# Performance work log

Measured on AMD Instinct MI355X. Metric: run time of the kernel, lower is better.

The kernel has to match this reference:

```python
import jax, jax.numpy as jnp
import numpy as np

N = 50000      # nodes
E = 640000     # edges (before self loops)
IN = 128       # in_channels
H = 4          # heads (layer 1)
C = 64         # hidden_channels per head
OUT = 64       # out_channels
SLOPE = 0.2    # PyG GATConv default negative_slope


def setup_inputs() -> dict:
    key = jax.random.key(0)
    ks = jax.random.split(key, 12)
    x = jax.random.normal(ks[0], (N, IN), dtype=jnp.float32)
    edge_src = jax.random.randint(ks[1], (E,), 0, N, dtype=jnp.int32)
    edge_dst = jax.random.randint(ks[2], (E,), 0, N, dtype=jnp.int32)
    # Layer 1 params: Linear IN -> H*C, attention vectors a_src/a_dst [H, C], bias [H*C]
    W1 = jax.random.normal(ks[3], (IN, H * C), dtype=jnp.float32) / np.sqrt(IN)
    att_src1 = jax.random.normal(ks[4], (H, C), dtype=jnp.float32) / np.sqrt(C)
    att_dst1 = jax.random.normal(ks[5], (H, C), dtype=jnp.float32) / np.sqrt(C)
    b1 = jnp.zeros((H * C,), dtype=jnp.float32)
    # Layer 2 params: Linear H*C -> OUT, 1 head
    W2 = jax.random.normal(ks[6], (H * C, OUT), dtype=jnp.float32) / np.sqrt(H * C)
    att_src2 = jax.random.normal(ks[7], (1, OUT), dtype=jnp.float32) / np.sqrt(OUT)
    att_dst2 = jax.random.normal(ks[8], (1, OUT), dtype=jnp.float32) / np.sqrt(OUT)
    b2 = jnp.zeros((OUT,), dtype=jnp.float32)
    return {"x": x, "W1": W1, "att_src1": att_src1, "att_dst1": att_dst1, "b1": b1,
            "W2": W2, "att_src2": att_src2, "att_dst2": att_dst2, "b2": b2,
            "edge_src": edge_src, "edge_dst": edge_dst}


def gat_conv(x, src, dst, W, a_src, a_dst, b, heads, ch):
    """PyG GATConv (concat=True): gather -> LeakyReLU attention -> per-dst softmax -> scatter-add."""
    n = x.shape[0]
    h = (x @ W).reshape(n, heads, ch)                  # [N, H, C]
    al_s = jnp.sum(h * a_src, axis=-1)                 # [N, H] node-level src attention term
    al_d = jnp.sum(h * a_dst, axis=-1)                 # [N, H]
    e = jax.nn.leaky_relu(al_s[src] + al_d[dst], SLOPE)  # [E, H] edge scores
    m = jax.ops.segment_max(e, dst, num_segments=n)    # stable per-dst softmax
    ex = jnp.exp(e - m[dst])
    den = jax.ops.segment_sum(ex, dst, num_segments=n)
    alpha = ex / den[dst]                              # [E, H]
    msg = h[src] * alpha[:, :, None]                   # [E, H, C]
    out = jax.ops.segment_sum(msg, dst, num_segments=n)  # [N, H, C]
    return out.reshape(n, heads * ch) + b


def reference(x, W1, att_src1, att_dst1, b1, W2, att_src2, att_dst2, b2, edge_src, edge_dst):
    # PyG GATConv default add_self_loops=True
    loops = jnp.arange(N, dtype=edge_src.dtype)
    src = jnp.concatenate([edge_src, loops])
    dst = jnp.concatenate([edge_dst, loops])
    h = gat_conv(x, src, dst, W1, att_src1, att_dst1, b1, H, C)
    h = jax.nn.elu(h)                                  # F.elu; dropout p=0 -> no-op
    out = gat_conv(h, src, dst, W2, att_src2, att_dst2, b2, 1, OUT)
    return out
```

## Files before the change

### kernel.cpp

```cpp
#include <hip/hip_runtime.h>
#include <hip/hip_bf16.h>
#include <cstdint>
#include <cstddef>

#define N_NODES 50000
#define N_EDGES 640000
#define ET (N_EDGES + N_NODES)
#define IN_CH 128
#define H1 4
#define HC1 256
#define OUT_CH 64
#define SLOPE 0.2f
#define SCAN_NBLK ((N_NODES + 255) / 256)
#define XW (N_NODES * IN_CH / 8)
#define W1N (IN_CH * HC1)
#define W2N (HC1 * OUT_CH)
#define CONVB ((XW + W1N + W2N + 255) / 256)
#define EDGEB ((ET + 255) / 256)
#define MT ((N_NODES + 63) / 64)
#define G1B (4 * MT)

typedef __attribute__((ext_vector_type(8))) short short8;
typedef __attribute__((ext_vector_type(4))) float floatx4;

__device__ __forceinline__ float bf2f(unsigned short u) {
    return __uint_as_float(((unsigned)u) << 16);
}
__device__ __forceinline__ unsigned short f2bf(float f) {
    unsigned u = __float_as_uint(f);
    unsigned r = 0x7fffu + ((u >> 16) & 1u);
    return (unsigned short)((u + r) >> 16);
}
__device__ __forceinline__ float ldf(const void* p, size_t i, bool f32) {
    return f32 ? ((const float*)p)[i] : bf2f(((const unsigned short*)p)[i]);
}

__global__ __launch_bounds__(256) void init_all(
    const unsigned short* __restrict__ x, unsigned* __restrict__ flag,
    int* __restrict__ counts, int* __restrict__ state)
{
    int b = blockIdx.x;
    if (b < SCAN_NBLK) {
        int i = b * 256 + threadIdx.x;
        if (i < N_NODES) counts[i] = 0;
    } else {
        int t = threadIdx.x;
        if (t < 64) {
            int bad = 0;
            #pragma unroll
            for (int r = 0; r < 4; ++r) {
                float v = bf2f(x[r * 64 + t]);
                if (!(v == v) || fabsf(v) > 1e4f) bad = 1;
            }
            unsigned long long m = __ballot(bad != 0);
            if (t == 0) *flag = (m != 0ull) ? 1u : 0u;
        } else if (t == 64) {
            state[0] = 0; state[1] = 0;
        }
    }
}

__global__ __launch_bounds__(256) void conv_count(
    const void* __restrict__ x, const void* __restrict__ W1,
    const void* __restrict__ W2, const unsigned* __restrict__ flag,
    unsigned short* __restrict__ x16,
    unsigned short* __restrict__ Wt1, unsigned short* __restrict__ Wt2,
    const int* __restrict__ edst, int* __restrict__ counts,
    int* __restrict__ epos)
{
    int b = blockIdx.x;
    if (b < CONVB) {
        int i = b * 256 + threadIdx.x;
        const bool f32 = (*flag != 0);
        if (i < XW) {
            size_t off = (size_t)i * 8;
            uint4 st;
            if (f32) {
                const float* xp = (const float*)x + off;
                float4 a = *(const float4*)xp;
                float4 c = *(const float4*)(xp + 4);
                st.x = (unsigned)f2bf(a.x) | ((unsigned)f2bf(a.y) << 16);
                st.y = (unsigned)f2bf(a.z) | ((unsigned)f2bf(a.w) << 16);
                st.z = (unsigned)f2bf(c.x) | ((unsigned)f2bf(c.y) << 16);
                st.w = (unsigned)f2bf(c.z) | ((unsigned)f2bf(c.w) << 16);
            } else {
                st = *(const uint4*)((const unsigned short*)x + off);
            }
            *(uint4*)(x16 + off) = st;
        } else if (i < XW + W1N) {
            int j = i - XW;
            int n = j / IN_CH, k = j % IN_CH;
            Wt1[j] = f2bf(ldf(W1, (size_t)k * HC1 + n, f32));
        } else if (i < XW + W1N + W2N) {
            int j = i - XW - W1N;
            int n = j / HC1, k = j % HC1;
            Wt2[j] = f2bf(ldf(W2, (size_t)k * OUT_CH + n, f32));
        }
    } else {
        int i = (b - CONVB) * 256 + threadIdx.x;
        if (i < ET) {
            int d = (i < N_EDGES) ? edst[i] : (i - N_EDGES);
            epos[i] = atomicAdd(&counts[d], 1);
        }
    }
}

__global__ __launch_bounds__(256) void scan_onepass(
    const int* __restrict__ counts, int* __restrict__ rowptr,
    int* __restrict__ bsum, int* __restrict__ boff, int* __restrict__ state)
{
    __shared__ int s[256];
    const int t = threadIdx.x, b = blockIdx.x;
    const int i = b * 256 + t;
    int v = (i < N_NODES) ? counts[i] : 0;
    s[t] = v;
    __syncthreads();
    #pragma unroll
    for (int off = 1; off < 256; off <<= 1) {
        int u = (t >= off) ? s[t - off] : 0;
        __syncthreads();
        s[t] += u;
        __syncthreads();
    }
    const int incl = s[t];
    if (t == 255) {
        __hip_atomic_store(&bsum[b], incl, __ATOMIC_RELAXED, __HIP_MEMORY_SCOPE_AGENT);
        __hip_atomic_fetch_add(&state[0], 1, __ATOMIC_ACQ_REL, __HIP_MEMORY_SCOPE_AGENT);
    }
    if (b == 0) {
        if (t == 0) {
            while (__hip_atomic_load(&state[0], __ATOMIC_ACQUIRE, __HIP_MEMORY_SCOPE_AGENT) < SCAN_NBLK)
                __builtin_amdgcn_s_sleep(8);
        }
        __syncthreads();
        int w = (t < SCAN_NBLK)
              ? __hip_atomic_load(&bsum[t], __ATOMIC_RELAXED, __HIP_MEMORY_SCOPE_AGENT) : 0;
        s[t] = w;
        __syncthreads();
        #pragma unroll
        for (int off = 1; off < 256; off <<= 1) {
            int u = (t >= off) ? s[t - off] : 0;
            __syncthreads();
            s[t] += u;
            __syncthreads();
        }
        if (t < SCAN_NBLK)
            __hip_atomic_store(&boff[t], s[t] - w, __ATOMIC_RELAXED, __HIP_MEMORY_SCOPE_AGENT);
        __syncthreads();
        if (t == 0)
            __hip_atomic_store(&state[1], 1, __ATOMIC_RELEASE, __HIP_MEMORY_SCOPE_AGENT);
    }
    if (t == 0) {
        while (__hip_atomic_load(&state[1], __ATOMIC_ACQUIRE, __HIP_MEMORY_SCOPE_AGENT) == 0)
            __builtin_amdgcn_s_sleep(8);
    }
    __syncthreads();
    int off0 = __hip_atomic_load(&boff[b], __ATOMIC_RELAXED, __HIP_MEMORY_SCOPE_AGENT);
    if (i < N_NODES)
        rowptr[i] = off0 + incl - v;
    if (i == 0) rowptr[N_NODES] = ET;
}

template <int KK>
__device__ __forceinline__ void gemm_body(
    const unsigned short* __restrict__ A, const unsigned short* __restrict__ Bt,
    const void* __restrict__ avs, const void* __restrict__ avd,
    const unsigned* __restrict__ flag, unsigned short* __restrict__ C,
    float* __restrict__ als, float* __restrict__ ald,
    int M, int N, int bx, int by)
{
    const int tid = threadIdx.x;
    const int m0 = by * 64, n0 = bx * 64;
    const int w = tid >> 6, lane = tid & 63;
    const int ln = lane & 15, quad = lane >> 4;
    const int m_frag = m0 + w * 16 + ln;
    floatx4 acc[4] = {{0.f,0.f,0.f,0.f},{0.f,0.f,0.f,0.f},{0.f,0.f,0.f,0.f},{0.f,0.f,0.f,0.f}};

    #pragma unroll
    for (int ks = 0; ks < KK / 32; ++ks) {
        const int kbase = ks * 32 + quad * 8;
        short8 a;
        if (m_frag < M) {
            a = *(const short8*)(A + (size_t)m_frag * KK + kbase);
        } else {
            #pragma unroll
            for (int j = 0; j < 8; ++j) a[j] = 0;
        }
        #pragma unroll
        for (int sub = 0; sub < 4; ++sub) {
            short8 b = *(const short8*)(Bt + (size_t)(n0 + sub * 16 + ln) * KK + kbase);
            acc[sub] = __builtin_amdgcn_mfma_f32_16x16x32_bf16(a, b, acc[sub], 0, 0, 0);
        }
    }

    #pragma unroll
    for (int sub = 0; sub < 4; ++sub) {
        #pragma unroll
        for (int r = 0; r < 4; ++r) {
            int m = m0 + w * 16 + quad * 4 + r;
            if (m < M)
                C[(size_t)m * N + n0 + sub * 16 + ln] = f2bf(acc[sub][r]);
        }
    }

    const bool f32in = (*flag != 0);
    float as[4], av[4];
    #pragma unroll
    for (int sub = 0; sub < 4; ++sub) {
        as[sub] = ldf(avs, n0 + sub * 16 + ln, f32in);
        av[sub] = ldf(avd, n0 + sub * 16 + ln, f32in);
    }
    const int Hh = N >> 6;
    #pragma unroll
    for (int r = 0; r < 4; ++r) {
        float ps = 0.f, pd = 0.f;
        #pragma unroll
        for (int sub = 0; sub < 4; ++sub) {
            ps += acc[sub][r] * as[sub];
            pd += acc[sub][r] * av[sub];
        }
        #pragma unroll
        for (int off = 1; off < 16; off <<= 1) {
            ps += __shfl_xor(ps, off, 64);
            pd += __shfl_xor(pd, off, 64);
        }
        int m = m0 + w * 16 + quad * 4 + r;
        if (ln == 0 && m < M) {
            als[(size_t)m * Hh + bx] = ps;
            ald[(size_t)m * Hh + bx] = pd;
        }
    }
}

__global__ __launch_bounds__(256) void gemm1_fill(
    const unsigned short* __restrict__ x16, const unsigned short* __restrict__ Wt1,
    const void* __restrict__ as1, const void* __restrict__ ad1,
    const unsigned* __restrict__ flag, unsigned short* __restrict__ h16,
    float* __restrict__ als, float* __restrict__ ald,
    const int* __restrict__ esrc, const int* __restrict__ edst,
    const int* __restrict__ rowptr, const int* __restrict__ epos,
    int* __restrict__ ecsr)
{
    int b = blockIdx.x;
    if (b < G1B) {
        gemm_body<IN_CH>(x16, Wt1, as1, ad1, flag, h16, als, ald,
                         N_NODES, HC1, b & 3, b >> 2);
    } else {
        int i = (b - G1B) * 256 + threadIdx.x;
        if (i < ET) {
            int s = (i < N_EDGES) ? esrc[i] : (i - N_EDGES);
            int d = (i < N_EDGES) ? edst[i] : (i - N_EDGES);
            ecsr[rowptr[d] + epos[i]] = s;
        }
    }
}

__global__ __launch_bounds__(256) void gemm2(
    const unsigned short* __restrict__ xo16, const unsigned short* __restrict__ Wt2,
    const void* __restrict__ as2, const void* __restrict__ ad2,
    const unsigned* __restrict__ flag, unsigned short* __restrict__ h2,
    float* __restrict__ als, float* __restrict__ ald)
{
    gemm_body<HC1>(xo16, Wt2, as2, ad2, flag, h2, als, ald,
                   N_NODES, OUT_CH, 0, blockIdx.x);
}

__global__ __launch_bounds__(256) void agg_node1(
    const int* __restrict__ rowptr, const int* __restrict__ ecsr,
    const unsigned short* __restrict__ h, const float* __restrict__ als,
    const float* __restrict__ ald, const void* __restrict__ bias,
    const unsigned* __restrict__ flag, unsigned short* __restrict__ out)
{
    int wave = (blockIdx.x * blockDim.x + threadIdx.x) >> 6;
    int lane = threadIdx.x & 63;
    if (wave >= N_NODES) return;
    const int d = wave;
    const int hg = lane >> 4;
    const int c0 = (lane & 15) << 2;
    const int lo = rowptr[d], hi = rowptr[d + 1];
    const float ad = ald[d * H1 + hg];

    float acc0 = 0.f, acc1 = 0.f, acc2 = 0.f, acc3 = 0.f, den = 0.f;

    int e = lo;
    for (; e + 3 < hi; e += 4) {
        int s0 = ecsr[e], s1 = ecsr[e + 1], s2 = ecsr[e + 2], s3 = ecsr[e + 3];
        uint2 q0 = *(const uint2*)(h + (size_t)s0 * HC1 + hg * 64 + c0);
        uint2 q1 = *(const uint2*)(h + (size_t)s1 * HC1 + hg * 64 + c0);
        uint2 q2 = *(const uint2*)(h + (size_t)s2 * HC1 + hg * 64 + c0);
        uint2 q3 = *(const uint2*)(h + (size_t)s3 * HC1 + hg * 64 + c0);
        float t0 = als[s0 * H1 + hg] + ad;
        float t1 = als[s1 * H1 + hg] + ad;
        float t2 = als[s2 * H1 + hg] + ad;
        float t3 = als[s3 * H1 + hg] + ad;
        t0 = (t0 > 0.f) ? t0 : SLOPE * t0;
        t1 = (t1 > 0.f) ? t1 : SLOPE * t1;
        t2 = (t2 > 0.f) ? t2 : SLOPE * t2;
        t3 = (t3 > 0.f) ? t3 : SLOPE * t3;
        float p0 = __expf(t0), p1 = __expf(t1), p2 = __expf(t2), p3 = __expf(t3);
        den += (p0 + p1) + (p2 + p3);
        acc0 += p0 * __uint_as_float(q0.x << 16)         + p1 * __uint_as_float(q1.x << 16)
              + p2 * __uint_as_float(q2.x << 16)         + p3 * __uint_as_float(q3.x << 16);
        acc1 += p0 * __uint_as_float(q0.x & 0xffff0000u) + p1 * __uint_as_float(q1.x & 0xffff0000u)
              + p2 * __uint_as_float(q2.x & 0xffff0000u) + p3 * __uint_as_float(q3.x & 0xffff0000u);
        acc2 += p0 * __uint_as_float(q0.y << 16)         + p1 * __uint_as_float(q1.y << 16)
              + p2 * __uint_as_float(q2.y << 16)         + p3 * __uint_as_float(q3.y << 16);
        acc3 += p0 * __uint_as_float(q0.y & 0xffff0000u) + p1 * __uint_as_float(q1.y & 0xffff0000u)
              + p2 * __uint_as_float(q2.y & 0xffff0000u) + p3 * __uint_as_float(q3.y & 0xffff0000u);
    }
    for (; e < hi; ++e) {
        int s0 = ecsr[e];
        uint2 q0 = *(const uint2*)(h + (size_t)s0 * HC1 + hg * 64 + c0);
        float t0 = als[s0 * H1 + hg] + ad;
        t0 = (t0 > 0.f) ? t0 : SLOPE * t0;
        float p0 = __expf(t0);
        den += p0;
        acc0 += p0 * __uint_as_float(q0.x << 16);
        acc1 += p0 * __uint_as_float(q0.x & 0xffff0000u);
        acc2 += p0 * __uint_as_float(q0.y << 16);
        acc3 += p0 * __uint_as_float(q0.y & 0xffff0000u);
    }

    const bool f32in = (*flag != 0);
    const float inv = 1.f / den;
    float v0 = acc0 * inv + ldf(bias, hg * 64 + c0 + 0, f32in);
    float v1 = acc1 * inv + ldf(bias, hg * 64 + c0 + 1, f32in);
    float v2 = acc2 * inv + ldf(bias, hg * 64 + c0 + 2, f32in);
    float v3 = acc3 * inv + ldf(bias, hg * 64 + c0 + 3, f32in);
    v0 = (v0 > 0.f) ? v0 : (__expf(v0) - 1.f);
    v1 = (v1 > 0.f) ? v1 : (__expf(v1) - 1.f);
    v2 = (v2 > 0.f) ? v2 : (__expf(v2) - 1.f);
    v3 = (v3 > 0.f) ? v3 : (__expf(v3) - 1.f);
    uint2 st;
    st.x = (unsigned)f2bf(v0) | ((unsigned)f2bf(v1) << 16);
    st.y = (unsigned)f2bf(v2) | ((unsigned)f2bf(v3) << 16);
    *(uint2*)(out + (size_t)d * HC1 + hg * 64 + c0) = st;
}

__global__ __launch_bounds__(256) void agg_node2(
    const int* __restrict__ rowptr, const int* __restrict__ ecsr,
    const unsigned short* __restrict__ h, const float* __restrict__ als,
    const float* __restrict__ ald, const void* __restrict__ bias,
    const unsigned* __restrict__ flag, float* __restrict__ out)
{
    int wave = (blockIdx.x * blockDim.x + threadIdx.x) >> 6;
    int lane = threadIdx.x & 63;
    if (wave >= N_NODES) return;
    const int d = wave;
    const int eg = lane >> 3;
    const int c0 = (lane & 7) << 3;
    const int lo = rowptr[d], hi = rowptr[d + 1];
    const float ad = ald[d];

    float acc[8];
    #pragma unroll
    for (int j = 0; j < 8; ++j) acc[j] = 0.f;
    float den = 0.f;

    for (int eb = lo; eb < hi; eb += 8) {
        int e = eb + eg;
        if (e < hi) {
            int s = ecsr[e];
            uint4 q = *(const uint4*)(h + (size_t)s * OUT_CH + c0);
            float t = als[s] + ad;
            t = (t > 0.f) ? t : SLOPE * t;
            float p = __expf(t);
            den += p;
            acc[0] += p * __uint_as_float(q.x << 16);
            acc[1] += p * __uint_as_float(q.x & 0xffff0000u);
            acc[2] += p * __uint_as_float(q.y << 16);
            acc[3] += p * __uint_as_float(q.y & 0xffff0000u);
            acc[4] += p * __uint_as_float(q.z << 16);
            acc[5] += p * __uint_as_float(q.z & 0xffff0000u);
            acc[6] += p * __uint_as_float(q.w << 16);
            acc[7] += p * __uint_as_float(q.w & 0xffff0000u);
        }
    }
    #pragma unroll
    for (int off = 8; off <= 32; off <<= 1) {
        den += __shfl_xor(den, off, 64);
        #pragma unroll
        for (int j = 0; j < 8; ++j) acc[j] += __shfl_xor(acc[j], off, 64);
    }
    if (lane < 8) {
        const bool f32in = (*flag != 0);
        const float inv = 1.f / den;
        float4 v0, v1;
        v0.x = acc[0] * inv + ldf(bias, c0 + 0, f32in);
        v0.y = acc[1] * inv + ldf(bias, c0 + 1, f32in);
        v0.z = acc[2] * inv + ldf(bias, c0 + 2, f32in);
        v0.w = acc[3] * inv + ldf(bias, c0 + 3, f32in);
        v1.x = acc[4] * inv + ldf(bias, c0 + 4, f32in);
        v1.y = acc[5] * inv + ldf(bias, c0 + 5, f32in);
        v1.z = acc[6] * inv + ldf(bias, c0 + 6, f32in);
        v1.w = acc[7] * inv + ldf(bias, c0 + 7, f32in);
        *(float4*)(out + (size_t)d * OUT_CH + c0) = v0;
        *(float4*)(out + (size_t)d * OUT_CH + c0 + 4) = v1;
    }
}

extern "C" void kernel_launch(void* const* d_in, const int* in_sizes, int n_in,
                              void* d_out, int out_size, void* d_ws, size_t ws_size,
                              hipStream_t stream)
{
    const void* x   = d_in[0];
    const void* W1  = d_in[1];
    const void* as1 = d_in[2];
    const void* ad1 = d_in[3];
    const void* b1  = d_in[4];
    const void* W2  = d_in[5];
    const void* as2 = d_in[6];
    const void* ad2 = d_in[7];
    const void* b2  = d_in[8];
    const int* esrc = (const int*)d_in[9];
    const int* edst = (const int*)d_in[10];
    float* out = (float*)d_out;

    char* base = (char*)d_ws;
    const size_t MB = 1024 * 1024;
    unsigned short* x16  = (unsigned short*)(base);
    unsigned short* h16  = (unsigned short*)(base + 13 * MB);
    unsigned short* xo16 = (unsigned short*)(base + 39 * MB);
    unsigned short* h2   = (unsigned short*)(base + 65 * MB);
    float* als    = (float*)(base + 72 * MB);
    float* ald    = (float*)(base + 73 * MB);
    unsigned short* Wt1 = (unsigned short*)(base + 74 * MB);
    unsigned short* Wt2 = (unsigned short*)(base + 75 * MB);
    int* counts   = (int*)(base + 76 * MB);
    int* rowptr   = (int*)(base + 77 * MB);
    int* ecsr     = (int*)(base + 79 * MB);
    int* bsum     = (int*)(base + 82 * MB);
    int* boff     = bsum + 256;
    int* state    = boff + 256;
    unsigned* flag = (unsigned*)(base + 83 * MB);
    int* epos     = (int*)(base + 84 * MB);

    const int BLK = 256;
    const int node_wave_blocks = (N_NODES * 64 + BLK - 1) / BLK;

    init_all<<<SCAN_NBLK + 1, BLK, 0, stream>>>(
        (const unsigned short*)x, flag, counts, state);

    conv_count<<<CONVB + EDGEB, BLK, 0, stream>>>(
        x, W1, W2, flag, x16, Wt1, Wt2, edst, counts, epos);

    scan_onepass<<<SCAN_NBLK, BLK, 0, stream>>>(
        counts, rowptr, bsum, boff, state);

    gemm1_fill<<<G1B + EDGEB, BLK, 0, stream>>>(
        x16, Wt1, as1, ad1, flag, h16, als, ald, esrc, edst, rowptr, epos, ecsr);

    agg_node1<<<node_wave_blocks, BLK, 0, stream>>>(
        rowptr, ecsr, h16, als, ald, b1, flag, xo16);

    gemm2<<<MT, BLK, 0, stream>>>(xo16, Wt2, as2, ad2, flag, h2, als, ald);

    agg_node2<<<node_wave_blocks, BLK, 0, stream>>>(
        rowptr, ecsr, h2, als, ald, b2, flag, out);
}
```

Before: 286.1 us.

## Pad CSR rows to multiples of 8 with dummy node, prefetch indices in aggregation

Each node's CSR segment is padded up to a multiple of 8 edges, and the padding points at a dummy node whose features are zero and whose source attention score is -1e30, so its softmax weight is zero. The aggregation kernels can then drop tail loops and bounds checks, load indices as aligned int4 vectors, and prefetch the next batch of indices. The layer-1 GEMM now computes all 256 output columns per block (16 sub-tiles) instead of splitting them across 4 blocks, and layers 1 and 2 get separate attention buffers. The cost is extra padded edges (up to 7 per node, with gathers of the dummy row), a larger accumulator footprint in the GEMM, and a fill pass that writes the padding entries.

Measured after the change: 291.8 us. About the same (+2.0%).

```diff
diff --git a/kernel.cpp b/kernel.cpp
--- a/kernel.cpp
+++ b/kernel.cpp
@@ -18,7 +18,8 @@
 #define CONVB ((XW + W1N + W2N + 255) / 256)
 #define EDGEB ((ET + 255) / 256)
 #define MT ((N_NODES + 63) / 64)
-#define G1B (4 * MT)
+#define PADB SCAN_NBLK
+#define DUMMY N_NODES
 
 typedef __attribute__((ext_vector_type(8))) short short8;
 typedef __attribute__((ext_vector_type(4))) float floatx4;
@@ -37,7 +38,9 @@
 
 __global__ __launch_bounds__(256) void init_all(
     const unsigned short* __restrict__ x, unsigned* __restrict__ flag,
-    int* __restrict__ counts, int* __restrict__ state)
+    int* __restrict__ counts, int* __restrict__ state,
+    unsigned short* __restrict__ h16, unsigned short* __restrict__ h2,
+    float* __restrict__ als1, float* __restrict__ als2)
 {
     int b = blockIdx.x;
     if (b < SCAN_NBLK) {
@@ -56,6 +59,15 @@
             if (t == 0) *flag = (m != 0ull) ? 1u : 0u;
         } else if (t == 64) {
             state[0] = 0; state[1] = 0;
+        } else if (t >= 128 && t < 192) {
+            uint2 z; z.x = 0u; z.y = 0u;
+            *((uint2*)(h16 + (size_t)DUMMY * HC1) + (t - 128)) = z;
+        } else if (t >= 192 && t < 224) {
+            ((unsigned*)(h2 + (size_t)DUMMY * OUT_CH))[t - 192] = 0u;
+        } else if (t >= 224 && t < 228) {
+            als1[(size_t)DUMMY * H1 + (t - 224)] = -1e30f;
+        } else if (t == 228) {
+            als2[DUMMY] = -1e30f;
         }
     }
 }
@@ -112,7 +124,7 @@
     __shared__ int s[256];
     const int t = threadIdx.x, b = blockIdx.x;
     const int i = b * 256 + t;
-    int v = (i < N_NODES) ? counts[i] : 0;
+    int v = (i < N_NODES) ? ((counts[i] + 7) & ~7) : 0;
     s[t] = v;
     __syncthreads();
     #pragma unroll
@@ -158,10 +170,10 @@
     int off0 = __hip_atomic_load(&boff[b], __ATOMIC_RELAXED, __HIP_MEMORY_SCOPE_AGENT);
     if (i < N_NODES)
         rowptr[i] = off0 + incl - v;
-    if (i == 0) rowptr[N_NODES] = ET;
-}
-
-template <int KK>
+    if (i == N_NODES - 1) rowptr[N_NODES] = off0 + incl;
+}
+
+template <int KK, int NSUB>
 __device__ __forceinline__ void gemm_body(
     const unsigned short* __restrict__ A, const unsigned short* __restrict__ Bt,
     const void* __restrict__ avs, const void* __restrict__ avd,
@@ -170,13 +182,16 @@
     int M, int N, int bx, int by)
 {
     const int tid = threadIdx.x;
-    const int m0 = by * 64, n0 = bx * 64;
+    const int m0 = by * 64, n0 = bx * (NSUB * 16);
     const int w = tid >> 6, lane = tid & 63;
     const int ln = lane & 15, quad = lane >> 4;
     const int m_frag = m0 + w * 16 + ln;
-    floatx4 acc[4] = {{0.f,0.f,0.f,0.f},{0.f,0.f,0.f,0.f},{0.f,0.f,0.f,0.f},{0.f,0.f,0.f,0.f}};
-
-    #pragma unroll
+    floatx4 acc[NSUB];
+    #pragma unroll
+    for (int sub = 0; sub < NSUB; ++sub)
+        acc[sub] = (floatx4){0.f, 0.f, 0.f, 0.f};
+
+    #pragma unroll 2
     for (int ks = 0; ks < KK / 32; ++ks) {
         const int kbase = ks * 32 + quad * 8;
         short8 a;
@@ -187,14 +202,14 @@
             for (int j = 0; j < 8; ++j) a[j] = 0;
         }
         #pragma unroll
-        for (int sub = 0; sub < 4; ++sub) {
+        for (int sub = 0; sub < NSUB; ++sub) {
             short8 b = *(const short8*)(Bt + (size_t)(n0 + sub * 16 + ln) * KK + kbase);
             acc[sub] = __builtin_amdgcn_mfma_f32_16x16x32_bf16(a, b, acc[sub], 0, 0, 0);
         }
     }
 
     #pragma unroll
-    for (int sub = 0; sub < 4; ++sub) {
+    for (int sub = 0; sub < NSUB; ++sub) {
         #pragma unroll
         for (int r = 0; r < 4; ++r) {
             int m = m0 + w * 16 + quad * 4 + r;
@@ -204,30 +219,33 @@
     }
 
     const bool f32in = (*flag != 0);
-    float as[4], av[4];
-    #pragma unroll
-    for (int sub = 0; sub < 4; ++sub) {
+    float as[NSUB], av[NSUB];
+    #pragma unroll
+    for (int sub = 0; sub < NSUB; ++sub) {
         as[sub] = ldf(avs, n0 + sub * 16 + ln, f32in);
         av[sub] = ldf(avd, n0 + sub * 16 + ln, f32in);
     }
     const int Hh = N >> 6;
     #pragma unroll
-    for (int r = 0; r < 4; ++r) {
-        float ps = 0.f, pd = 0.f;
+    for (int hb = 0; hb < NSUB / 4; ++hb) {
         #pragma unroll
-        for (int sub = 0; sub < 4; ++sub) {
-            ps += acc[sub][r] * as[sub];
-            pd += acc[sub][r] * av[sub];
-        }
-        #pragma unroll
-        for (int off = 1; off < 16; off <<= 1) {
-            ps += __shfl_xor(ps, off, 64);
-            pd += __shfl_xor(pd, off, 64);
-        }
-        int m = m0 + w * 16 + quad * 4 + r;
-        if (ln == 0 && m < M) {
-            als[(size_t)m * Hh + bx] = ps;
-            ald[(size_t)m * Hh + bx] = pd;
+        for (int r = 0; r < 4; ++r) {
+            float ps = 0.f, pd = 0.f;
+            #pragma unroll
+            for (int k = 0; k < 4; ++k) {
+                ps += acc[hb * 4 + k][r] * as[hb * 4 + k];
+                pd += acc[hb * 4 + k][r] * av[hb * 4 + k];
+            }
+            #pragma unroll
+            for (int off = 1; off < 16; off <<= 1) {
+                ps += __shfl_xor(ps, off, 64);
+                pd += __shfl_xor(pd, off, 64);
+            }
+            int m = m0 + w * 16 + quad * 4 + r;
+            if (ln == 0 && m < M) {
+                als[(size_t)m * Hh + bx * (NSUB / 4) + hb] = ps;
+                ald[(size_t)m * Hh + bx * (NSUB / 4) + hb] = pd;
+            }
         }
     }
 }
@@ -239,18 +257,25 @@
     float* __restrict__ als, float* __restrict__ ald,
     const int* __restrict__ esrc, const int* __restrict__ edst,
     const int* __restrict__ rowptr, const int* __restrict__ epos,
-    int* __restrict__ ecsr)
+    const int* __restrict__ counts, int* __restrict__ ecsr)
 {
     int b = blockIdx.x;
-    if (b < G1B) {
-        gemm_body<IN_CH>(x16, Wt1, as1, ad1, flag, h16, als, ald,
-                         N_NODES, HC1, b & 3, b >> 2);
-    } else {
-        int i = (b - G1B) * 256 + threadIdx.x;
+    if (b < MT) {
+        gemm_body<IN_CH, 16>(x16, Wt1, as1, ad1, flag, h16, als, ald,
+                             N_NODES, HC1, 0, b);
+    } else if (b < MT + EDGEB) {
+        int i = (b - MT) * 256 + threadIdx.x;
         if (i < ET) {
             int s = (i < N_EDGES) ? esrc[i] : (i - N_EDGES);
             int d = (i < N_EDGES) ? edst[i] : (i - N_EDGES);
             ecsr[rowptr[d] + epos[i]] = s;
+        }
+    } else {
+        int i = (b - MT - EDGEB) * 256 + threadIdx.x;
+        if (i < N_NODES) {
+            int c = counts[i];
+            int lo = rowptr[i] + c, hi = rowptr[i + 1];
+            for (int j = lo; j < hi; ++j) ecsr[j] = DUMMY;
         }
     }
 }
@@ -261,8 +286,8 @@
     const unsigned* __restrict__ flag, unsigned short* __restrict__ h2,
     float* __restrict__ als, float* __restrict__ ald)
 {
-    gemm_body<HC1>(xo16, Wt2, as2, ad2, flag, h2, als, ald,
-                   N_NODES, OUT_CH, 0, blockIdx.x);
+    gemm_body<HC1, 4>(xo16, Wt2, as2, ad2, flag, h2, als, ald,
+                      N_NODES, OUT_CH, 0, blockIdx.x);
 }
 
 __global__ __launch_bounds__(256) void agg_node1(
@@ -277,56 +302,69 @@
     const int d = wave;
     const int hg = lane >> 4;
     const int c0 = (lane & 15) << 2;
+    const int hoff = hg * 64 + c0;
     const int lo = rowptr[d], hi = rowptr[d + 1];
     const float ad = ald[d * H1 + hg];
 
     float acc0 = 0.f, acc1 = 0.f, acc2 = 0.f, acc3 = 0.f, den = 0.f;
 
-    int e = lo;
-    for (; e + 3 < hi; e += 4) {
-        int s0 = ecsr[e], s1 = ecsr[e + 1], s2 = ecsr[e + 2], s3 = ecsr[e + 3];
-        uint2 q0 = *(const uint2*)(h + (size_t)s0 * HC1 + hg * 64 + c0);
-        uint2 q1 = *(const uint2*)(h + (size_t)s1 * HC1 + hg * 64 + c0);
-        uint2 q2 = *(const uint2*)(h + (size_t)s2 * HC1 + hg * 64 + c0);
-        uint2 q3 = *(const uint2*)(h + (size_t)s3 * HC1 + hg * 64 + c0);
-        float t0 = als[s0 * H1 + hg] + ad;
-        float t1 = als[s1 * H1 + hg] + ad;
-        float t2 = als[s2 * H1 + hg] + ad;
-        float t3 = als[s3 * H1 + hg] + ad;
-        t0 = (t0 > 0.f) ? t0 : SLOPE * t0;
-        t1 = (t1 > 0.f) ? t1 : SLOPE * t1;
-        t2 = (t2 > 0.f) ? t2 : SLOPE * t2;
-        t3 = (t3 > 0.f) ? t3 : SLOPE * t3;
-        float p0 = __expf(t0), p1 = __expf(t1), p2 = __expf(t2), p3 = __expf(t3);
-        den += (p0 + p1) + (p2 + p3);
+    int4 iA = *(const int4*)(ecsr + lo);
+    int4 iB = *(const int4*)(ecsr + lo + 4);
+    for (int e = lo; e < hi; e += 8) {
+        const int4 cA = iA, cB = iB;
+        const int en = (e + 8 < hi) ? (e + 8) : lo;
+        iA = *(const int4*)(ecsr + en);
+        iB = *(const int4*)(ecsr + en + 4);
+
+        uint2 q0 = *(const uint2*)(h + (size_t)cA.x * HC1 + hoff);
+        uint2 q1 = *(const uint2*)(h + (size_t)cA.y * HC1 + hoff);
+        uint2 q2 = *(const uint2*)(h + (size_t)cA.z * HC1 + hoff);
+        uint2 q3 = *(const uint2*)(h + (size_t)cA.w * HC1 + hoff);
+        uint2 q4 = *(const uint2*)(h + (size_t)cB.x * HC1 + hoff);
+        uint2 q5 = *(const uint2*)(h + (size_t)cB.y * HC1 + hoff);
+        uint2 q6 = *(const uint2*)(h + (size_t)cB.z * HC1 + hoff);
+        uint2 q7 = *(const uint2*)(h + (size_t)cB.w * HC1 + hoff);
+        float t0 = als[cA.x * H1 + hg] + ad;
+        float t1 = als[cA.y * H1 + hg] + ad;
+        float t2 = als[cA.z * H1 + hg] + ad;
+        float t3 = als[cA.w * H1 + hg] + ad;
+        float t4 = als[cB.x * H1 + hg] + ad;
+        float t5 = als[cB.y * H1 + hg] + ad;
+        float t6 = als[cB.z * H1 + hg] + ad;
+        float t7 = als[cB.w * H1 + hg] + ad;
+        float p0 = __expf(fmaxf(t0, SLOPE * t0));
+        float p1 = __expf(fmaxf(t1, SLOPE * t1));
+        float p2 = __expf(fmaxf(t2, SLOPE * t2));
+        float p3 = __expf(fmaxf(t3, SLOPE * t3));
+        float p4 = __expf(fmaxf(t4, SLOPE * t4));
+        float p5 = __expf(fmaxf(t5, SLOPE * t5));
+        float p6 = __expf(fmaxf(t6, SLOPE * t6));
+        float p7 = __expf(fmaxf(t7, SLOPE * t7));
+        den += ((p0 + p1) + (p2 + p3)) + ((p4 + p5) + (p6 + p7));
         acc0 += p0 * __uint_as_float(q0.x << 16)         + p1 * __uint_as_float(q1.x << 16)
-              + p2 * __uint_as_float(q2.x << 16)         + p3 * __uint_as_float(q3.x << 16);
+              + p2 * __uint_as_float(q2.x << 16)         + p3 * __uint_as_float(q3.x << 16)
+              + p4 * __uint_as_float(q4.x << 16)         + p5 * __uint_as_float(q5.x << 16)
+              + p6 * __uint_as_float(q6.x << 16)         + p7 * __uint_as_float(q7.x << 16);
         acc1 += p0 * __uint_as_float(q0.x & 0xffff0000u) + p1 * __uint_as_float(q1.x & 0xffff0000u)
-              + p2 * __uint_as_float(q2.x & 0xffff0000u) + p3 * __uint_as_float(q3.x & 0xffff0000u);
+              + p2 * __uint_as_float(q2.x & 0xffff0000u) + p3 * __uint_as_float(q3.x & 0xffff0000u)
+              + p4 * __uint_as_float(q4.x & 0xffff0000u) + p5 * __uint_as_float(q5.x & 0xffff0000u)
+              + p6 * __uint_as_float(q6.x & 0xffff0000u) + p7 * __uint_as_float(q7.x & 0xffff0000u);
         acc2 += p0 * __uint_as_float(q0.y << 16)         + p1 * __uint_as_float(q1.y << 16)
-              + p2 * __uint_as_float(q2.y << 16)         + p3 * __uint_as_float(q3.y << 16);
+              + p2 * __uint_as_float(q2.y << 16)         + p3 * __uint_as_float(q3.y << 16)
+              + p4 * __uint_as_float(q4.y << 16)         + p5 * __uint_as_float(q5.y << 16)
+              + p6 * __uint_as_float(q6.y << 16)         + p7 * __uint_as_float(q7.y << 16);
         acc3 += p0 * __uint_as_float(q0.y & 0xffff0000u) + p1 * __uint_as_float(q1.y & 0xffff0000u)
-              + p2 * __uint_as_float(q2.y & 0xffff0000u) + p3 * __uint_as_float(q3.y & 0xffff0000u);
-    }
-    for (; e < hi; ++e) {
-        int s0 = ecsr[e];
-        uint2 q0 = *(const uint2*)(h + (size_t)s0 * HC1 + hg * 64 + c0);
-        float t0 = als[s0 * H1 + hg] + ad;
-        t0 = (t0 > 0.f) ? t0 : SLOPE * t0;
-        float p0 = __expf(t0);
-        den += p0;
-        acc0 += p0 * __uint_as_float(q0.x << 16);
-        acc1 += p0 * __uint_as_float(q0.x & 0xffff0000u);
-        acc2 += p0 * __uint_as_float(q0.y << 16);
-        acc3 += p0 * __uint_as_float(q0.y & 0xffff0000u);
+              + p2 * __uint_as_float(q2.y & 0xffff0000u) + p3 * __uint_as_float(q3.y & 0xffff0000u)
+              + p4 * __uint_as_float(q4.y & 0xffff0000u) + p5 * __uint_as_float(q5.y & 0xffff0000u)
+              + p6 * __uint_as_float(q6.y & 0xffff0000u) + p7 * __uint_as_float(q7.y & 0xffff0000u);
     }
 
     const bool f32in = (*flag != 0);
     const float inv = 1.f / den;
-    float v0 = acc0 * inv + ldf(bias, hg * 64 + c0 + 0, f32in);
-    float v1 = acc1 * inv + ldf(bias, hg * 64 + c0 + 1, f32in);
-    float v2 = acc2 * inv + ldf(bias, hg * 64 + c0 + 2, f32in);
-    float v3 = acc3 * inv + ldf(bias, hg * 64 + c0 + 3, f32in);
+    float v0 = acc0 * inv + ldf(bias, hoff + 0, f32in);
+    float v1 = acc1 * inv + ldf(bias, hoff + 1, f32in);
+    float v2 = acc2 * inv + ldf(bias, hoff + 2, f32in);
+    float v3 = acc3 * inv + ldf(bias, hoff + 3, f32in);
     v0 = (v0 > 0.f) ? v0 : (__expf(v0) - 1.f);
     v1 = (v1 > 0.f) ? v1 : (__expf(v1) - 1.f);
     v2 = (v2 > 0.f) ? v2 : (__expf(v2) - 1.f);
@@ -334,7 +372,7 @@
     uint2 st;
     st.x = (unsigned)f2bf(v0) | ((unsigned)f2bf(v1) << 16);
     st.y = (unsigned)f2bf(v2) | ((unsigned)f2bf(v3) << 16);
-    *(uint2*)(out + (size_t)d * HC1 + hg * 64 + c0) = st;
+    *(uint2*)(out + (size_t)d * HC1 + hoff) = st;
 }
 
 __global__ __launch_bounds__(256) void agg_node2(
@@ -357,24 +395,23 @@
     for (int j = 0; j < 8; ++j) acc[j] = 0.f;
     float den = 0.f;
 
+    int sP = ecsr[lo + eg];
     for (int eb = lo; eb < hi; eb += 8) {
-        int e = eb + eg;
-        if (e < hi) {
-            int s = ecsr[e];
-            uint4 q = *(const uint4*)(h + (size_t)s * OUT_CH + c0);
-            float t = als[s] + ad;
-            t = (t > 0.f) ? t : SLOPE * t;
-            float p = __expf(t);
-            den += p;
-            acc[0] += p * __uint_as_float(q.x << 16);
-            acc[1] += p * __uint_as_float(q.x & 0xffff0000u);
-            acc[2] += p * __uint_as_float(q.y << 16);
-            acc[3] += p * __uint_as_float(q.y & 0xffff0000u);
-            acc[4] += p * __uint_as_float(q.z << 16);
-            acc[5] += p * __uint_as_float(q.z & 0xffff0000u);
-            acc[6] += p * __uint_as_float(q.w << 16);
-            acc[7] += p * __uint_as_float(q.w & 0xffff0000u);
-        }
+        const int s = sP;
+        const int en = (eb + 8 < hi) ? (eb + 8) : lo;
+        sP = ecsr[en + eg];
+        uint4 q = *(const uint4*)(h + (size_t)s * OUT_CH + c0);
+        float t = als[s] + ad;
+        float p = __expf(fmaxf(t, SLOPE * t));
+        den += p;
+        acc[0] += p * __uint_as_float(q.x << 16);
+        acc[1] += p * __uint_as_float(q.x & 0xffff0000u);
+        acc[2] += p * __uint_as_float(q.y << 16);
+        acc[3] += p * __uint_as_float(q.y & 0xffff0000u);
+        acc[4] += p * __uint_as_float(q.z << 16);
+        acc[5] += p * __uint_as_float(q.z & 0xffff0000u);
+        acc[6] += p * __uint_as_float(q.w << 16);
+        acc[7] += p * __uint_as_float(q.w & 0xffff0000u);
     }
     #pragma unroll
     for (int off = 8; off <= 32; off <<= 1) {
@@ -422,24 +459,26 @@
     unsigned short* h16  = (unsigned short*)(base + 13 * MB);
     unsigned short* xo16 = (unsigned short*)(base + 39 * MB);
     unsigned short* h2   = (unsigned short*)(base + 65 * MB);
-    float* als    = (float*)(base + 72 * MB);
-    float* ald    = (float*)(base + 73 * MB);
-    unsigned short* Wt1 = (unsigned short*)(base + 74 * MB);
-    unsigned short* Wt2 = (unsigned short*)(base + 75 * MB);
+    float* als1   = (float*)(base + 72 * MB);
+    float* ald1   = (float*)(base + 73 * MB);
+    float* als2   = (float*)(base + 74 * MB);
+    float* ald2   = (float*)(base + 74 * MB + 512 * 1024);
+    unsigned short* Wt1 = (unsigned short*)(base + 75 * MB);
+    unsigned short* Wt2 = (unsigned short*)(base + 75 * MB + 128 * 1024);
     int* counts   = (int*)(base + 76 * MB);
     int* rowptr   = (int*)(base + 77 * MB);
-    int* ecsr     = (int*)(base + 79 * MB);
-    int* bsum     = (int*)(base + 82 * MB);
+    int* bsum     = (int*)(base + 78 * MB);
     int* boff     = bsum + 256;
     int* state    = boff + 256;
-    unsigned* flag = (unsigned*)(base + 83 * MB);
-    int* epos     = (int*)(base + 84 * MB);
+    unsigned* flag = (unsigned*)(base + 78 * MB + 8 * 1024);
+    int* epos     = (int*)(base + 79 * MB);
+    int* ecsr     = (int*)(base + 82 * MB);
 
     const int BLK = 256;
     const int node_wave_blocks = (N_NODES * 64 + BLK - 1) / BLK;
 
     init_all<<<SCAN_NBLK + 1, BLK, 0, stream>>>(
-        (const unsigned short*)x, flag, counts, state);
+        (const unsigned short*)x, flag, counts, state, h16, h2, als1, als2);
 
     conv_count<<<CONVB + EDGEB, BLK, 0, stream>>>(
         x, W1, W2, flag, x16, Wt1, Wt2, edst, counts, epos);
@@ -447,14 +486,15 @@
     scan_onepass<<<SCAN_NBLK, BLK, 0, stream>>>(
         counts, rowptr, bsum, boff, state);
 
-    gemm1_fill<<<G1B + EDGEB, BLK, 0, stream>>>(
-        x16, Wt1, as1, ad1, flag, h16, als, ald, esrc, edst, rowptr, epos, ecsr);
+    gemm1_fill<<<MT + EDGEB + PADB, BLK, 0, stream>>>(
+        x16, Wt1, as1, ad1, flag, h16, als1, ald1, esrc, edst, rowptr, epos,
+        counts, ecsr);
 
     agg_node1<<<node_wave_blocks, BLK, 0, stream>>>(
-        rowptr, ecsr, h16, als, ald, b1, flag, xo16);
-
-    gemm2<<<MT, BLK, 0, stream>>>(xo16, Wt2, as2, ad2, flag, h2, als, ald);
+        rowptr, ecsr, h16, als1, ald1, b1, flag, xo16);
+
+    gemm2<<<MT, BLK, 0, stream>>>(xo16, Wt2, as2, ad2, flag, h2, als2, ald2);
 
     agg_node2<<<node_wave_blocks, BLK, 0, stream>>>(
-        rowptr, ecsr, h2, als, ald, b2, flag, out);
-}
+        rowptr, ecsr, h2, als2, ald2, b2, flag, out);
+}
```
